# Kernel optimization log

Hardware: AMD Instinct MI355X
Metric: run time of the kernel (lower is better)

Reference implementation:

```python
import jax, jax.numpy as jnp
import numpy as np

C = 256            # in_channels
SHIFTS = (1, 2, 3, 4)
S = len(SHIFTS)
HID = C // S       # 64
H = W = 64
AREA = H * W
EPS = 1e-5
NORM_EPS = 1e-12
# offsets (dy, dx) encoded by the 8 one-hot 3x3 kernels (kernels 1..8)
OFFSETS = [(-1,-1), (-1,0), (-1,1), (0,1), (1,1), (1,0), (1,-1), (0,-1)]


def shift2d(x, dy, dx):
    # x: [b, c, H, W]; out[y, x] = x[y+dy, x+dx], zeros outside (== dilated depthwise conv with one-hot kernel)
    d = max(abs(dy), abs(dx), 1)
    xp = jnp.pad(x, ((0,0),(0,0),(d,d),(d,d)))
    return xp[:, :, d+dy:d+dy+x.shape[2], d+dx:d+dx+x.shape[3]]


def setup_inputs() -> dict:
    key = jax.random.key(0)
    ks = jax.random.split(key, 8)
    sd = 0.02
    return {
        "cen": jax.random.normal(ks[0], (4, C, H, W), dtype=jnp.float32),
        "query_w": jax.random.normal(ks[1], (S, HID, C), dtype=jnp.float32) * sd,
        "local_w": jax.random.normal(ks[2], (S, HID, C), dtype=jnp.float32) * sd,
        "key_w":   jax.random.normal(ks[3], (S, 8*HID, 8*C), dtype=jnp.float32) * sd,
        "value_w": jax.random.normal(ks[4], (S, 8*HID, 8*C), dtype=jnp.float32) * sd,
        "out_w":   jax.random.normal(ks[5], (C, C), dtype=jnp.float32) * sd,
        "bn_gamma": jnp.ones((C,), dtype=jnp.float32),
        "bn_beta":  jnp.zeros((C,), dtype=jnp.float32),
    }


def reference(cen, query_w, local_w, key_w, value_w, out_w, bn_gamma, bn_beta):
    b, _, h, w = cen.shape
    cenf = cen.reshape(b, C, AREA)
    keys, qs, vals, locs = [], [], [], []
    for i, d in enumerate(SHIFTS):
        # gather 8 dilated neighbors -> [b, 8C, area]
        surr = jnp.concatenate([shift2d(cen, dy*d, dx*d) for dy, dx in OFFSETS], axis=1)
        surr = surr.reshape(b, 8*C, AREA)
        keys.append(jnp.einsum('oc,bca->boa', key_w[i], surr))
        vals.append(jnp.einsum('oc,bca->boa', value_w[i], surr))
        qs.append(jnp.einsum('oc,bca->boa', query_w[i], cenf))
        locs.append(jnp.einsum('oc,bca->boa', local_w[i], cenf))
    keys = jnp.stack(keys, 1)   # [b,S,8h,area]
    vals = jnp.stack(vals, 1)   # [b,S,8h,area]
    qs   = jnp.stack(qs, 1)     # [b,S,h,area]
    locs = jnp.stack(locs, 1)   # [b,S,h,area]

    # L2 normalize over area (torch F.normalize: x / max(||x||, eps))
    kn = keys / jnp.maximum(jnp.linalg.norm(keys, axis=-1, keepdims=True), NORM_EPS)
    qn = qs   / jnp.maximum(jnp.linalg.norm(qs,   axis=-1, keepdims=True), NORM_EPS)

    # channel attention: contract over area -> [b,S,h,8h]
    score = jnp.einsum('bsha,bska->bshk', qn, kn)
    # InstanceNorm2d over (h, 8h) per (b, S), affine=False, biased var
    mu = score.mean(axis=(-2,-1), keepdims=True)
    var = score.var(axis=(-2,-1), keepdims=True)
    score = (score - mu) * jax.lax.rsqrt(var + EPS)
    ws = jax.nn.softmax(score, axis=-1)                     # [b,S,h,8h]
    wc = ws.reshape(b, S, HID, 8, HID).sum(axis=3)          # sum of 8 chunks -> [b,S,h,h]

    out = jnp.einsum('bshk,bska->bsha', ws, vals) - jnp.einsum('bshk,bska->bsha', wc, locs)
    out = out.reshape(b, C, h, w)

    # out_conv: 1x1 conv -> BatchNorm2d (training stats, biased var) -> ReLU
    out = jnp.einsum('oc,bchw->bohw', out_w, out)
    m = out.mean(axis=(0,2,3), keepdims=True)
    v = out.var(axis=(0,2,3), keepdims=True)
    out = (out - m) * jax.lax.rsqrt(v + EPS)
    out = out * bn_gamma[None, :, None, None] + bn_beta[None, :, None, None]
    return jax.nn.relu(out)
```

## Files before the change

kernel.cpp:

```cpp
#include <hip/hip_runtime.h>


typedef unsigned short u16;
typedef unsigned int u32;
typedef __attribute__((ext_vector_type(4))) unsigned int u32x4;
typedef __attribute__((ext_vector_type(8))) short s16x8;
typedef __attribute__((ext_vector_type(4))) float f32x4;

#define DEVFN static __device__ __forceinline__

DEVFN u16 f2bf(float f) {
    u32 u = __builtin_bit_cast(u32, f);
    u32 r = (u + 0x7fffu + ((u >> 16) & 1u)) >> 16;
    return (u16)r;
}
DEVFN float bf2f(u32 h) { u32 u = h << 16; return __builtin_bit_cast(float, u); }

typedef __attribute__((address_space(1))) const unsigned int gu32;
typedef __attribute__((address_space(3))) unsigned int lu32;
DEVFN void gld16(const void* g, void* l) {
    __builtin_amdgcn_global_load_lds((gu32*)g, (lu32*)l, 16, 0, 0);
}

__constant__ int cOFFY[8] = {-1,-1,-1, 0, 1, 1, 1, 0};
__constant__ int cOFFX[8] = {-1, 0, 1, 1, 1, 0,-1,-1};

#define CENROWS 4097

DEVFN int swz(int r, int kb) { return r * 128 + (kb ^ ((r & 7) << 4)); }

template<int BM, int BN, int WRM, int WRN, int XG, int YG, int DM, int NRM, int KSP, int SWZ>
__global__ __launch_bounds__(256, 2)
void gemm_tn(const u16* __restrict__ X, const u16* __restrict__ Y,
             void* __restrict__ D, const u16* __restrict__ cenT,
             float* __restrict__ nrm,
             int K, int ldx, int ldy, int ldd, int sbits,
             long xb, long xs, long yb, long ys, long db, long dsn,
             long nb, long ns, long kpl)
{
    static_assert(KSP == 1 || (!XG && !YG), "split-K only for non-gather");
    int bx = blockIdx.x, by = blockIdx.y, bz = blockIdx.z;
    if constexpr (SWZ) {
        const int gx = gridDim.x, gy = gridDim.y;
        const int nwg = gx * gy * (int)gridDim.z;
        const int flat = bx + gx * (by + gy * bz);
        const int r = (flat & 7) * (nwg >> 3) + (flat >> 3);
        bx = r % gx; by = (r / gx) % gy; bz = r / (gx * gy);
    }
    const int tid  = threadIdx.x;
    const int lane = tid & 63;
    const int wid  = tid >> 6;
    const int b = bz >> sbits;
    const int s = bz & ((1 << sbits) - 1);
    const int m0 = bx * BM;
    const int ksl = (KSP > 1) ? (by % KSP) : 0;
    const int n0 = (KSP > 1 ? (by / KSP) : by) * BN;
    const int koff = ksl * (K / KSP);
    const int dil = s + 1;
    const int wm0 = (wid >> 1) * (WRM * 16);
    const int wn0 = (wid & 1) * (WRN * 16);

    __shared__ __align__(16) char lds[2 * (BM + BN) * 128];

    const char* cenB = (const char*)(cenT + (long)b * (CENROWS * 256));
    const char* Xb = nullptr;
    const char* Yb = nullptr;
    if constexpr (!XG) Xb = (const char*)(X + b * xb + (long)s * xs + (long)m0 * ldx + koff);
    if constexpr (!YG) Yb = (const char*)(Y + b * yb + (long)s * ys + (long)n0 * ldy + koff);

    u32 offX[XG ? BM / 32 : 1];
    u32 offY[YG ? BN / 32 : 1];
    auto calcOff = [&](int j) {
        const int dy = (j < 8) ? cOFFY[j] * dil : 0;
        const int dx = (j < 8) ? cOFFX[j] * dil : 0;
        if constexpr (XG) {
            #pragma unroll
            for (int r = 0; r < BM / 32; r++) {
                const int R = r * 32 + wid * 8 + (lane >> 3);
                const int a = m0 + R, yy = (a >> 6) + dy, xx = (a & 63) + dx;
                const int row = (((unsigned)yy < 64u) && ((unsigned)xx < 64u)) ? ((yy << 6) + xx) : 4096;
                offX[r] = ((u32)row << 9) + (((lane & 7) * 16) ^ ((R & 7) << 4));
            }
        }
        if constexpr (YG) {
            #pragma unroll
            for (int r = 0; r < BN / 32; r++) {
                const int R = r * 32 + wid * 8 + (lane >> 3);
                const int a = n0 + R, yy = (a >> 6) + dy, xx = (a & 63) + dx;
                const int row = (((unsigned)yy < 64u) && ((unsigned)xx < 64u)) ? ((yy << 6) + xx) : 4096;
                offY[r] = ((u32)row << 9) + (((lane & 7) * 16) ^ ((R & 7) << 4));
            }
        }
    };

    auto stage = [&](int bf, int t) {
        char* LX = lds + bf * ((BM + BN) * 128);
        char* LY = LX + BM * 128;
        if constexpr (!XG) {
            const char* base = Xb + (long)t * 128;
            #pragma unroll
            for (int r = 0; r < BM / 32; r++) {
                const int R = r * 32 + wid * 8 + (lane >> 3);
                gld16(base + (long)R * (ldx * 2) + (((lane & 7) * 16) ^ ((R & 7) << 4)),
                      LX + (r * 32 + wid * 8) * 128);
            }
        } else {
            const int cb = (t & 3) * 128;
            #pragma unroll
            for (int r = 0; r < BM / 32; r++)
                gld16(cenB + offX[r] + cb, LX + (r * 32 + wid * 8) * 128);
        }
        if constexpr (!YG) {
            const char* base = Yb + (long)t * 128;
            #pragma unroll
            for (int r = 0; r < BN / 32; r++) {
                const int R = r * 32 + wid * 8 + (lane >> 3);
                gld16(base + (long)R * (ldy * 2) + (((lane & 7) * 16) ^ ((R & 7) << 4)),
                      LY + (r * 32 + wid * 8) * 128);
            }
        } else {
            const int cb = (t & 3) * 128;
            #pragma unroll
            for (int r = 0; r < BN / 32; r++)
                gld16(cenB + offY[r] + cb, LY + (r * 32 + wid * 8) * 128);
        }
    };

    f32x4 acc[WRM][WRN] = {};

    auto comp = [&](int bf) {
        const char* LX = lds + bf * ((BM + BN) * 128);
        const char* LY = LX + BM * 128;
        #pragma unroll
        for (int kk = 0; kk < 2; kk++) {
            const int kb = kk * 64 + ((lane >> 4) << 4);
            s16x8 af[WRM], bfr[WRN];
            #pragma unroll
            for (int m = 0; m < WRM; m++)
                af[m] = *(const s16x8*)(LX + swz(wm0 + m * 16 + (lane & 15), kb));
            #pragma unroll
            for (int n = 0; n < WRN; n++)
                bfr[n] = *(const s16x8*)(LY + swz(wn0 + n * 16 + (lane & 15), kb));
            #pragma unroll
            for (int m = 0; m < WRM; m++)
                #pragma unroll
                for (int n = 0; n < WRN; n++)
                    acc[m][n] = __builtin_amdgcn_mfma_f32_16x16x32_bf16(af[m], bfr[n], acc[m][n], 0, 0, 0);
        }
    };

    const int nt = (K / KSP) / 64;
    if constexpr (XG || YG) calcOff(0);
    stage(0, 0);
    __syncthreads();
    int cur = 0;
    for (int t = 0; t < nt; t++) {
        if (t + 1 < nt) {
            if constexpr (XG || YG) {
                if (((t + 1) & 3) == 0) calcOff((t + 1) >> 2);
            }
            stage(cur ^ 1, t + 1);
        }
        comp(cur);
        __syncthreads();
        cur ^= 1;
    }

    if constexpr (NRM) {
        const int slot = (by << 1) + (wid & 1);
        #pragma unroll
        for (int m = 0; m < WRM; m++) {
            float ss[4] = {0.f, 0.f, 0.f, 0.f};
            float s1v[4] = {0.f, 0.f, 0.f, 0.f};
            #pragma unroll
            for (int n = 0; n < WRN; n++)
                #pragma unroll
                for (int i = 0; i < 4; i++) {
                    float v = (NRM == 1) ? bf2f(f2bf(acc[m][n][i])) : acc[m][n][i];
                    ss[i] += v * v;
                    if constexpr (NRM == 2) s1v[i] += v;
                }
            #pragma unroll
            for (int o = 1; o < 16; o <<= 1)
                #pragma unroll
                for (int i = 0; i < 4; i++) {
                    ss[i] += __shfl_xor(ss[i], o);
                    if constexpr (NRM == 2) s1v[i] += __shfl_xor(s1v[i], o);
                }
            if ((lane & 15) == 0) {
                const int row0 = m0 + wm0 + m * 16 + ((lane >> 4) << 2);
                #pragma unroll
                for (int i = 0; i < 4; i++) {
                    if constexpr (NRM == 1) {
                        nrm[((long)(b * nb + s * ns + row0 + i) << 6) + slot] = ss[i];
                    } else {
                        float* p = nrm + ((long)(row0 + i) << 8) + (b << 6) + slot;
                        p[0] = s1v[i];
                        p[65536] = ss[i];
                    }
                }
            }
        }
    }

    #pragma unroll
    for (int m = 0; m < WRM; m++) {
        const int row0 = m0 + wm0 + m * 16 + ((lane >> 4) << 2);
        #pragma unroll
        for (int n = 0; n < WRN; n++) {
            const int col = n0 + wn0 + n * 16 + (lane & 15);
            f32x4 a = acc[m][n];
            if constexpr (DM == 1) {
                float* Dp = (float*)D + (long)ksl * kpl + b * db + (long)s * dsn;
                #pragma unroll
                for (int i = 0; i < 4; i++) Dp[(long)(row0 + i) * ldd + col] = a[i];
            } else {
                u16* Dp = (u16*)D + b * db + (long)s * dsn;
                #pragma unroll
                for (int i = 0; i < 4; i++) Dp[(long)(row0 + i) * ldd + col] = f2bf(a[i]);
            }
        }
    }
}

__global__ void castbf(const float* __restrict__ src, u16* __restrict__ dst, int n8, float scale) {
    int i = blockIdx.x * 256 + threadIdx.x;
    if (i >= n8) return;
    const float* s = src + (long)i * 8;
    u32x4 o;
    #pragma unroll
    for (int j = 0; j < 4; j++) {
        u16 lo = f2bf(s[2 * j] * scale), hi = f2bf(s[2 * j + 1] * scale);
        o[j] = (u32)lo | ((u32)hi << 16);
    }
    *(u32x4*)(dst + (long)i * 8) = o;
}

__global__ __launch_bounds__(256) void zrow(u16* __restrict__ cenT) {
    const int b = blockIdx.x;
    u32* p = (u32*)(cenT + (long)b * (CENROWS * 256) + 4096L * 256);
    if (threadIdx.x < 128) p[threadIdx.x] = 0u;
}

__global__ __launch_bounds__(256) void transpose_cast(const float* __restrict__ src, u16* __restrict__ dst,
                                                      int R, int C, float scale, long dstride) {
    __shared__ float t[64][65];
    const int tx = threadIdx.x & 63, ty = threadIdx.x >> 6;
    const int c0 = blockIdx.x * 64, r0 = blockIdx.y * 64;
    const float* s = src + (long)blockIdx.z * R * C + (long)r0 * C + c0;
    #pragma unroll
    for (int i = 0; i < 16; i++) t[ty + i * 4][tx] = s[(long)(ty + i * 4) * C + tx];
    __syncthreads();
    u16* d = dst + (long)blockIdx.z * dstride + (long)c0 * R + r0;
    #pragma unroll
    for (int i = 0; i < 16; i++) d[(long)(ty + i * 4) * R + tx] = f2bf(t[tx][ty + i * 4] * scale);
}

__global__ __launch_bounds__(256) void softmax_in(const float* __restrict__ score,
                                                  const float* __restrict__ nQp,
                                                  const float* __restrict__ nKp,
                                                  u16* __restrict__ wswc) {
    constexpr long PL = 524288;
    const int bs = blockIdx.x, tid = threadIdx.x;
    const int b = bs >> 2, s = bs & 3;
    const float* S = score + (long)bs * 32768;
    __shared__ float invq[64], invk[512];
    if (tid < 64) {
        const float* p = nQp + ((long)(b * 256 + s * 64 + tid) << 6);
        float a = 0.f;
        #pragma unroll
        for (int j = 0; j < 64; j++) a += p[j];
        invq[tid] = 1.f / fmaxf(sqrtf(a), 1e-12f);
    }
    for (int i = tid; i < 512; i += 256) {
        const float* p = nKp + (((long)bs * 512 + i) << 6);
        float a = 0.f;
        #pragma unroll
        for (int j = 0; j < 64; j++) a += p[j];
        invk[i] = 1.f / fmaxf(sqrtf(a), 1e-12f);
    }
    __syncthreads();
    auto ldS = [&](int i) -> float {
        return S[i] + S[i + PL] + S[i + 2 * PL] + S[i + 3 * PL];
    };
    float s1 = 0.f, s2 = 0.f;
    for (int i = tid; i < 32768; i += 256) {
        float v = ldS(i) * invq[i >> 9] * invk[i & 511];
        s1 += v; s2 += v * v;
    }
    __shared__ float ra[256], rb[256];
    ra[tid] = s1; rb[tid] = s2; __syncthreads();
    for (int st = 128; st > 0; st >>= 1) {
        if (tid < st) { ra[tid] += ra[tid + st]; rb[tid] += rb[tid + st]; }
        __syncthreads();
    }
    const float mu = ra[0] * (1.f / 32768.f);
    const float var = rb[0] * (1.f / 32768.f) - mu * mu;
    const float rstd = rsqrtf(var + 1e-5f);
    const int wid = tid >> 6, lane = tid & 63;
    u16* W = wswc + (long)bs * 64 * 576;
    for (int r = wid; r < 64; r += 4) {
        float zv[8]; float mx = -3.0e38f;
        const float iq = invq[r];
        #pragma unroll
        for (int i = 0; i < 8; i++) {
            const int c = i * 64 + lane;
            zv[i] = (ldS(r * 512 + c) * iq * invk[c] - mu) * rstd;
            mx = fmaxf(mx, zv[i]);
        }
        #pragma unroll
        for (int o = 32; o > 0; o >>= 1) mx = fmaxf(mx, __shfl_xor(mx, o));
        float sum = 0.f;
        #pragma unroll
        for (int i = 0; i < 8; i++) { zv[i] = __expf(zv[i] - mx); sum += zv[i]; }
        #pragma unroll
        for (int o = 32; o > 0; o >>= 1) sum += __shfl_xor(sum, o);
        const float inv = 1.f / sum;
        float wcv = 0.f;
        #pragma unroll
        for (int i = 0; i < 8; i++) {
            float w = zv[i] * inv; wcv += w;
            W[r * 576 + i * 64 + lane] = f2bf(w);
        }
        W[r * 576 + 512 + lane] = f2bf(wcv);
    }
}

__global__ __launch_bounds__(256) void bn_finalize(const float* __restrict__ bnp,
                                                   const float* __restrict__ gamma,
                                                   const float* __restrict__ beta,
                                                   float* __restrict__ st) {
    const int c = threadIdx.x;
    const float* p = bnp + ((long)c << 8);
    float s1 = 0.f, s2 = 0.f;
    #pragma unroll 8
    for (int j = 0; j < 256; j++) { s1 += p[j]; s2 += p[65536 + j]; }
    const float mu = s1 * (1.f / 16384.f);
    const float var = s2 * (1.f / 16384.f) - mu * mu;
    const float g = gamma[c] * rsqrtf(var + 1e-5f);
    st[c * 2] = g;
    st[c * 2 + 1] = beta[c] - mu * g;
}

__global__ __launch_bounds__(256) void bn_apply(const u16* __restrict__ out2b,
                                                const float* __restrict__ st,
                                                float* __restrict__ out) {
    const long i8 = (long)blockIdx.x * 256 + threadIdx.x;
    const u32x4 v = *(const u32x4*)(out2b + i8 * 8);
    const int c = (int)((i8 * 8) >> 12) & 255;
    const float g = st[c * 2], bt = st[c * 2 + 1];
    float* o = out + i8 * 8;
    #pragma unroll
    for (int j = 0; j < 4; j++) {
        o[2 * j]     = fmaxf(bf2f(v[j] & 0xffff) * g + bt, 0.f);
        o[2 * j + 1] = fmaxf(bf2f(v[j] >> 16) * g + bt, 0.f);
    }
}

extern "C" void kernel_launch(void* const* d_in, const int* in_sizes, int n_in,
                              void* d_out, int out_size, void* d_ws, size_t ws_size,
                              hipStream_t stream) {
    (void)in_sizes; (void)n_in; (void)out_size; (void)ws_size;
    const float* cen   = (const float*)d_in[0];
    const float* qw    = (const float*)d_in[1];
    const float* lw    = (const float*)d_in[2];
    const float* kw    = (const float*)d_in[3];
    const float* vw    = (const float*)d_in[4];
    const float* ow    = (const float*)d_in[5];
    const float* gamma = (const float*)d_in[6];
    const float* beta  = (const float*)d_in[7];
    float* out = (float*)d_out;

    char* ws = (char*)d_ws;
    size_t off = 0;
    auto alloc = [&](size_t bytes) { size_t o = off; off += (bytes + 255) & ~(size_t)255; return o; };
    u16*   KWb   = (u16*)(ws + alloc(4L * 512 * 2048 * 2));
    u16*   VWt   = (u16*)(ws + alloc(4L * 2048 * 512 * 2));
    u16*   QWb   = (u16*)(ws + alloc(256L * 256 * 2));
    u16*   LWt   = (u16*)(ws + alloc(4L * 256 * 64 * 2));
    u16*   OWb   = (u16*)(ws + alloc(256L * 256 * 2));
    u16*   cenT  = (u16*)(ws + alloc(4L * CENROWS * 256 * 2));
    u16*   keys  = (u16*)(ws + alloc(16L * 512 * 4096 * 2));
    u16*   qs    = (u16*)(ws + alloc(16L * 64 * 4096 * 2));
    float* score = (float*)(ws + alloc(4L * 16 * 64 * 512 * 4));
    u16*   WSWC  = (u16*)(ws + alloc(16L * 64 * 576 * 2));
    u16*   Xcomb = (u16*)(ws + alloc(16L * 64 * 2304 * 2));
    u16*   out1t = (u16*)(ws + alloc(4L * 4096 * 256 * 2));
    u16*   out2b = (u16*)(ws + alloc(4L * 256 * 4096 * 2));
    float* bnst  = (float*)(ws + alloc(256L * 2 * 4));
    float* nKp   = (float*)(ws + alloc(16L * 512 * 64 * 4));
    float* nQp   = (float*)(ws + alloc(4L * 256 * 64 * 4));
    float* bnp   = (float*)(ws + alloc(2L * 65536 * 4));

    castbf<<<dim3(2048), 256, 0, stream>>>(kw, KWb, 524288, 1.f);
    castbf<<<dim3(32),   256, 0, stream>>>(qw, QWb, 8192, 1.f);
    castbf<<<dim3(32),   256, 0, stream>>>(ow, OWb, 8192, 1.f);
    transpose_cast<<<dim3(32, 8, 4), 256, 0, stream>>>(vw, VWt, 512, 2048, 1.f, 512L * 2048);
    transpose_cast<<<dim3(4, 1, 4),  256, 0, stream>>>(lw, LWt, 64, 256, -1.f, 64L * 256);
    transpose_cast<<<dim3(64, 4, 4), 256, 0, stream>>>(cen, cenT, 256, 4096, 1.f, (long)CENROWS * 256);
    zrow<<<dim3(4), 256, 0, stream>>>(cenT);

    gemm_tn<128,128,4,4, 0,1, 0, 1, 1, 1><<<dim3(4, 32, 16), 256, 0, stream>>>(
        KWb, nullptr, keys, cenT, nKp,
        2048, 2048, 0, 4096, 2,
        0L, 512L * 2048, 0L, 0L, 4L * 512 * 4096, 512L * 4096, 2048L, 512L, 0L);
    gemm_tn<128,128,4,4, 0,0, 0, 1, 1, 0><<<dim3(2, 32, 4), 256, 0, stream>>>(
        QWb, cenT, qs, cenT, nQp,
        256, 256, 256, 4096, 0,
        0L, 0L, (long)CENROWS * 256, 0L, 256L * 4096, 0L, 256L, 0L, 0L);
    gemm_tn<64,64,2,2, 0,0, 1, 0, 4, 0><<<dim3(1, 32, 16), 256, 0, stream>>>(
        qs, keys, score, cenT, nullptr,
        4096, 4096, 4096, 512, 2,
        256L * 4096, 64L * 4096, 4L * 512 * 4096, 512L * 4096, 4L * 64 * 512, 64L * 512,
        0L, 0L, 524288L);
    softmax_in<<<dim3(16), 256, 0, stream>>>(score, nQp, nKp, WSWC);

    gemm_tn<64,128,2,4, 0,0, 0, 0, 1, 0><<<dim3(1, 16, 16), 256, 0, stream>>>(
        WSWC, VWt, Xcomb, cenT, nullptr,
        512, 576, 512, 2304, 2,
        4L * 64 * 576, 64L * 576, 0L, 2048L * 512, 4L * 64 * 2304, 64L * 2304, 0L, 0L, 0L);
    gemm_tn<64,128,2,4, 0,0, 0, 0, 1, 0><<<dim3(1, 2, 16), 256, 0, stream>>>(
        WSWC + 512, LWt, Xcomb + 2048, cenT, nullptr,
        64, 576, 64, 2304, 2,
        4L * 64 * 576, 64L * 576, 0L, 256L * 64, 4L * 64 * 2304, 64L * 2304, 0L, 0L, 0L);
    gemm_tn<128,64,4,2, 1,0, 0, 0, 1, 1><<<dim3(32, 1, 16), 256, 0, stream>>>(
        nullptr, Xcomb, out1t, cenT, nullptr,
        2304, 0, 2304, 256, 2,
        0L, 0L, 4L * 64 * 2304, 64L * 2304, 4096L * 256, 64L, 0L, 0L, 0L);

    gemm_tn<128,128,4,4, 0,0, 0, 2, 1, 0><<<dim3(2, 32, 4), 256, 0, stream>>>(
        OWb, out1t, out2b, cenT, bnp,
        256, 256, 256, 4096, 0,
        0L, 0L, 4096L * 256, 0L, 256L * 4096, 0L, 0L, 0L, 0L);

    bn_finalize<<<dim3(1), 256, 0, stream>>>(bnp, gamma, beta, bnst);
    bn_apply<<<dim3(2048), 256, 0, stream>>>(out2b, bnst, out);
}
```

Baseline: 326.7 us.

## Merge weight casts and zero-row into one launch, widen softmax block, retile small GEMMs

Folds the three bf16 weight casts and the cenT zero-row kernel into a single launch to cut launch overhead. The softmax/instance-norm kernel now runs with 1024 threads per block instead of 256, so each of its 16 blocks has more parallelism. The query and output-conv GEMMs move from 128x128 to 64x128 tiles, doubling the grid to fill more CUs. The cost is larger reductions and shared arrays in softmax, and the zero-row write now shares a launch that must finish before the transpose writes cenT.

```diff
diff --git a/kernel.cpp b/kernel.cpp
--- a/kernel.cpp
+++ b/kernel.cpp
@@ -223,23 +223,31 @@
     }
 }
 
-__global__ void castbf(const float* __restrict__ src, u16* __restrict__ dst, int n8, float scale) {
-    int i = blockIdx.x * 256 + threadIdx.x;
-    if (i >= n8) return;
-    const float* s = src + (long)i * 8;
-    u32x4 o;
+__global__ void cast_all(const float* __restrict__ kw, const float* __restrict__ qw,
+                         const float* __restrict__ ow,
+                         u16* __restrict__ KWb, u16* __restrict__ QWb,
+                         u16* __restrict__ OWb, u16* __restrict__ cenT) {
+    const int i = blockIdx.x * 256 + threadIdx.x;
+    const float* src; u16* dst; long o;
+    if (i < 524288)      { src = kw; dst = KWb; o = i; }
+    else if (i < 532480) { src = qw; dst = QWb; o = i - 524288; }
+    else if (i < 540672) { src = ow; dst = OWb; o = i - 532480; }
+    else {
+        const int t = (i - 540672) * 1;
+        if (t < 512) {
+            const int b = t >> 7, w = t & 127;
+            ((u32*)(cenT + (long)b * (CENROWS * 256) + 4096L * 256))[w] = 0u;
+        }
+        return;
+    }
+    const float* s = src + o * 8;
+    u32x4 v;
     #pragma unroll
     for (int j = 0; j < 4; j++) {
-        u16 lo = f2bf(s[2 * j] * scale), hi = f2bf(s[2 * j + 1] * scale);
-        o[j] = (u32)lo | ((u32)hi << 16);
-    }
-    *(u32x4*)(dst + (long)i * 8) = o;
-}
-
-__global__ __launch_bounds__(256) void zrow(u16* __restrict__ cenT) {
-    const int b = blockIdx.x;
-    u32* p = (u32*)(cenT + (long)b * (CENROWS * 256) + 4096L * 256);
-    if (threadIdx.x < 128) p[threadIdx.x] = 0u;
+        u16 lo = f2bf(s[2 * j]), hi = f2bf(s[2 * j + 1]);
+        v[j] = (u32)lo | ((u32)hi << 16);
+    }
+    *(u32x4*)(dst + o * 8) = v;
 }
 
 __global__ __launch_bounds__(256) void transpose_cast(const float* __restrict__ src, u16* __restrict__ dst,
@@ -256,10 +264,10 @@
     for (int i = 0; i < 16; i++) d[(long)(ty + i * 4) * R + tx] = f2bf(t[tx][ty + i * 4] * scale);
 }
 
-__global__ __launch_bounds__(256) void softmax_in(const float* __restrict__ score,
-                                                  const float* __restrict__ nQp,
-                                                  const float* __restrict__ nKp,
-                                                  u16* __restrict__ wswc) {
+__global__ __launch_bounds__(1024) void softmax_in(const float* __restrict__ score,
+                                                   const float* __restrict__ nQp,
+                                                   const float* __restrict__ nKp,
+                                                   u16* __restrict__ wswc) {
     constexpr long PL = 524288;
     const int bs = blockIdx.x, tid = threadIdx.x;
     const int b = bs >> 2, s = bs & 3;
@@ -272,25 +280,25 @@
         for (int j = 0; j < 64; j++) a += p[j];
         invq[tid] = 1.f / fmaxf(sqrtf(a), 1e-12f);
     }
-    for (int i = tid; i < 512; i += 256) {
-        const float* p = nKp + (((long)bs * 512 + i) << 6);
+    if (tid < 512) {
+        const float* p = nKp + (((long)bs * 512 + tid) << 6);
         float a = 0.f;
         #pragma unroll
         for (int j = 0; j < 64; j++) a += p[j];
-        invk[i] = 1.f / fmaxf(sqrtf(a), 1e-12f);
+        invk[tid] = 1.f / fmaxf(sqrtf(a), 1e-12f);
     }
     __syncthreads();
     auto ldS = [&](int i) -> float {
         return S[i] + S[i + PL] + S[i + 2 * PL] + S[i + 3 * PL];
     };
     float s1 = 0.f, s2 = 0.f;
-    for (int i = tid; i < 32768; i += 256) {
+    for (int i = tid; i < 32768; i += 1024) {
         float v = ldS(i) * invq[i >> 9] * invk[i & 511];
         s1 += v; s2 += v * v;
     }
-    __shared__ float ra[256], rb[256];
+    __shared__ float ra[1024], rb[1024];
     ra[tid] = s1; rb[tid] = s2; __syncthreads();
-    for (int st = 128; st > 0; st >>= 1) {
+    for (int st = 512; st > 0; st >>= 1) {
         if (tid < st) { ra[tid] += ra[tid + st]; rb[tid] += rb[tid + st]; }
         __syncthreads();
     }
@@ -299,7 +307,7 @@
     const float rstd = rsqrtf(var + 1e-5f);
     const int wid = tid >> 6, lane = tid & 63;
     u16* W = wswc + (long)bs * 64 * 576;
-    for (int r = wid; r < 64; r += 4) {
+    for (int r = wid; r < 64; r += 16) {
         float zv[8]; float mx = -3.0e38f;
         const float iq = invq[r];
         #pragma unroll
@@ -392,19 +400,16 @@
     float* nQp   = (float*)(ws + alloc(4L * 256 * 64 * 4));
     float* bnp   = (float*)(ws + alloc(2L * 65536 * 4));
 
-    castbf<<<dim3(2048), 256, 0, stream>>>(kw, KWb, 524288, 1.f);
-    castbf<<<dim3(32),   256, 0, stream>>>(qw, QWb, 8192, 1.f);
-    castbf<<<dim3(32),   256, 0, stream>>>(ow, OWb, 8192, 1.f);
+    cast_all<<<dim3(2115), 256, 0, stream>>>(kw, qw, ow, KWb, QWb, OWb, cenT);
     transpose_cast<<<dim3(32, 8, 4), 256, 0, stream>>>(vw, VWt, 512, 2048, 1.f, 512L * 2048);
     transpose_cast<<<dim3(4, 1, 4),  256, 0, stream>>>(lw, LWt, 64, 256, -1.f, 64L * 256);
     transpose_cast<<<dim3(64, 4, 4), 256, 0, stream>>>(cen, cenT, 256, 4096, 1.f, (long)CENROWS * 256);
-    zrow<<<dim3(4), 256, 0, stream>>>(cenT);
 
     gemm_tn<128,128,4,4, 0,1, 0, 1, 1, 1><<<dim3(4, 32, 16), 256, 0, stream>>>(
         KWb, nullptr, keys, cenT, nKp,
         2048, 2048, 0, 4096, 2,
         0L, 512L * 2048, 0L, 0L, 4L * 512 * 4096, 512L * 4096, 2048L, 512L, 0L);
-    gemm_tn<128,128,4,4, 0,0, 0, 1, 1, 0><<<dim3(2, 32, 4), 256, 0, stream>>>(
+    gemm_tn<64,128,2,4, 0,0, 0, 1, 1, 0><<<dim3(4, 32, 4), 256, 0, stream>>>(
         QWb, cenT, qs, cenT, nQp,
         256, 256, 256, 4096, 0,
         0L, 0L, (long)CENROWS * 256, 0L, 256L * 4096, 0L, 256L, 0L, 0L);
@@ -413,7 +418,7 @@
         4096, 4096, 4096, 512, 2,
         256L * 4096, 64L * 4096, 4L * 512 * 4096, 512L * 4096, 4L * 64 * 512, 64L * 512,
         0L, 0L, 524288L);
-    softmax_in<<<dim3(16), 256, 0, stream>>>(score, nQp, nKp, WSWC);
+    softmax_in<<<dim3(16), 1024, 0, stream>>>(score, nQp, nKp, WSWC);
 
     gemm_tn<64,128,2,4, 0,0, 0, 0, 1, 0><<<dim3(1, 16, 16), 256, 0, stream>>>(
         WSWC, VWt, Xcomb, cenT, nullptr,
@@ -428,7 +433,7 @@
         2304, 0, 2304, 256, 2,
         0L, 0L, 4L * 64 * 2304, 64L * 2304, 4096L * 256, 64L, 0L, 0L, 0L);
 
-    gemm_tn<128,128,4,4, 0,0, 0, 2, 1, 0><<<dim3(2, 32, 4), 256, 0, stream>>>(
+    gemm_tn<64,128,2,4, 0,0, 0, 2, 1, 0><<<dim3(4, 32, 4), 256, 0, stream>>>(
         OWb, out1t, out2b, cenT, bnp,
         256, 256, 256, 4096, 0,
         0L, 0L, 4096L * 256, 0L, 256L * 4096, 0L, 0L, 0L, 0L);
```

Result: faster. 280.6 us (-14.1%).
